# Optimization experiments

Hardware: AMD Instinct MI355X
Metric: run time of the kernel (lower is better)

Reference implementation:

```python
import jax, jax.numpy as jnp
import numpy as np

QMAX = 127.0

def quantize_mat(mat):
    # per-row (last-dim) absmax scale, kept in fp16 like the torch code,
    # truncating cast to int8 (XLA float->int convert truncates toward zero, same as torch .to(int8))
    max_val = (jnp.max(jnp.abs(mat), axis=-1) / QMAX).astype(jnp.float16)
    q = (mat / max_val[..., None]).astype(jnp.int8)
    return q, max_val


def setup_inputs() -> dict:
    key = jax.random.key(0)
    k1, k2, k3, k4 = jax.random.split(key, 4)
    B, S, IN, OUT = 8, 4096, 2048, 2048
    x = jax.random.normal(k1, (B, S, IN), dtype=jnp.float16)
    ori_w = jax.random.normal(k2, (OUT, IN), dtype=jnp.float16)
    # SmoothQuant scales: positive, bounded away from 0 (torch clamps min=1e-5)
    scales = (jax.random.uniform(k3, (IN,), dtype=jnp.float16) + jnp.float16(0.5))
    bias = jax.random.normal(k4, (OUT,), dtype=jnp.float16)
    return {"x": x, "ori_w": ori_w, "scales": scales, "bias": bias}


def reference(x, ori_w, scales, bias):
    dtype = x.dtype
    # __init__-time: smooth the weight then quantize per output row
    w = (ori_w * scales).astype(dtype)                 # [OUT, IN]
    weight_q, w_max = quantize_mat(w)                  # int8 [OUT, IN], fp16 [OUT]
    weight_qt = weight_q.T                             # stored transposed [IN, OUT]
    # forward: smooth + quantize activations
    x = (x / scales).astype(dtype)                     # [B, S, IN]
    x_q, x_max = quantize_mat(x)                       # int8 [B,S,IN], fp16 [B,S]
    res_q = jnp.matmul(x_q.astype(jnp.float32), weight_qt.astype(jnp.float32))  # [B,S,OUT]
    # dequant factor: outer product of activation and weight scales (fp16 linear, then fp32)
    mx = (x_max[..., None] * w_max).astype(jnp.float32)  # [B,S,OUT]
    res = (res_q * mx).astype(dtype)
    res = res + bias
    return res
```

## Files before the change

kernel.cpp:

```cpp
#include <hip/hip_runtime.h>
#include <hip/hip_bf16.h>
#include <cstdint>
#include <cstddef>

#define M_TOT 32768
#define N_OUT 2048
#define K_IN  2048

typedef int v4i __attribute__((ext_vector_type(4)));

__device__ __forceinline__ void gload16(const int8_t* g, int8_t* l) {
  __builtin_amdgcn_global_load_lds(
      (const __attribute__((address_space(1))) void*)g,
      (__attribute__((address_space(3))) void*)l, 16, 0, 0);
}

__global__ __launch_bounds__(256) void quant_rows_kernel(
    const float* __restrict__ in,
    const float* __restrict__ scales,
    int8_t* __restrict__ q, float* __restrict__ rmax, int mul_mode)
{
  const int row = blockIdx.x;
  const int tid = threadIdx.x;
  const size_t base = (size_t)row * K_IN + tid * 8;
  const float4 xv0 = *(const float4*)(in + base);
  const float4 xv1 = *(const float4*)(in + base + 4);
  const float4 sv0 = *(const float4*)(scales + tid * 8);
  const float4 sv1 = *(const float4*)(scales + tid * 8 + 4);
  const float xf[8] = {xv0.x, xv0.y, xv0.z, xv0.w, xv1.x, xv1.y, xv1.z, xv1.w};
  const float sf[8] = {sv0.x, sv0.y, sv0.z, sv0.w, sv1.x, sv1.y, sv1.z, sv1.w};
  _Float16 xs[8];
  float amax = 0.f;
#pragma unroll
  for (int i = 0; i < 8; ++i) {
    const _Float16 hx = (_Float16)xf[i];
    const _Float16 hs = (_Float16)sf[i];
    xs[i] = mul_mode ? (_Float16)(hx * hs) : (_Float16)(hx / hs);
    amax = fmaxf(amax, fabsf((float)xs[i]));
  }
#pragma unroll
  for (int off = 32; off; off >>= 1) amax = fmaxf(amax, __shfl_down(amax, off));
  __shared__ float red[4];
  const int wid = tid >> 6, lane = tid & 63;
  if (lane == 0) red[wid] = amax;
  __syncthreads();
  amax = fmaxf(fmaxf(red[0], red[1]), fmaxf(red[2], red[3]));
  _Float16 hqm = (_Float16)amax / (_Float16)127.0f;
  if (tid == 0) rmax[row] = (float)hqm;
  if (hqm == (_Float16)0.f) hqm = (_Float16)1.0f;
  int8_t qb[8];
#pragma unroll
  for (int i = 0; i < 8; ++i) {
    const float qf = (float)(_Float16)(xs[i] / hqm);
    qb[i] = (int8_t)(int)qf;
  }
  unsigned long long pk;
  __builtin_memcpy(&pk, qb, 8);
  *(unsigned long long*)(q + (size_t)row * K_IN + tid * 8) = pk;
}

__global__ __launch_bounds__(256) void gemm_i8_kernel(
    const int8_t* __restrict__ Aq, const int8_t* __restrict__ Bq,
    const float* __restrict__ Am, const float* __restrict__ Bm,
    const float* __restrict__ bias, float* __restrict__ out)
{
  __shared__ int8_t sA[128 * 64];
  __shared__ int8_t sB[128 * 64];
  const int tid = threadIdx.x;
  const int wid = tid >> 6, lane = tid & 63;
  const int wm = wid >> 1, wn = wid & 1;
  const long bm = (long)blockIdx.y * 128;
  const long bn = (long)blockIdx.x * 128;

  const int srow = wid * 32 + (lane >> 2);
  const int scol = (((lane & 3) ^ ((lane >> 3) & 3))) * 16;
  const int8_t* ga = Aq + (bm + srow) * K_IN + scol;
  const int8_t* gb = Bq + (bn + srow) * K_IN + scol;
  int8_t* lA = sA + wid * 2048;
  int8_t* lB = sB + wid * 2048;

  const int fr = lane & 15, fq = lane >> 4;
  const int fp = (fq ^ ((fr >> 1) & 3)) * 16;
  const int8_t* ra = sA + (wm * 64 + fr) * 64 + fp;
  const int8_t* rb = sB + (wn * 64 + fr) * 64 + fp;

  v4i acc[4][4] = {};

  for (int kt = 0; kt < K_IN; kt += 64) {
    __syncthreads();
    gload16(ga + kt,             lA);
    gload16(ga + 16 * K_IN + kt, lA + 1024);
    gload16(gb + kt,             lB);
    gload16(gb + 16 * K_IN + kt, lB + 1024);
    __syncthreads();
    v4i a[4], b[4];
#pragma unroll
    for (int i = 0; i < 4; ++i) a[i] = *(const v4i*)(ra + i * 16 * 64);
#pragma unroll
    for (int i = 0; i < 4; ++i) b[i] = *(const v4i*)(rb + i * 16 * 64);
#pragma unroll
    for (int mi = 0; mi < 4; ++mi)
#pragma unroll
      for (int ni = 0; ni < 4; ++ni)
        acc[mi][ni] = __builtin_amdgcn_mfma_i32_16x16x64_i8(a[mi], b[ni], acc[mi][ni], 0, 0, 0);
  }

  const long cm0 = bm + wm * 64;
  const int  cn0 = (int)bn + wn * 64;
  float amv[4][4];
#pragma unroll
  for (int mi = 0; mi < 4; ++mi)
#pragma unroll
    for (int r = 0; r < 4; ++r)
      amv[mi][r] = Am[cm0 + mi * 16 + fq * 4 + r];
#pragma unroll
  for (int ni = 0; ni < 4; ++ni) {
    const int col = cn0 + ni * 16 + fr;
    const float wmv = Bm[col];
    const _Float16 bsv = (_Float16)bias[col];
#pragma unroll
    for (int mi = 0; mi < 4; ++mi) {
#pragma unroll
      for (int r = 0; r < 4; ++r) {
        const long row = cm0 + mi * 16 + fq * 4 + r;
        const float mx = (float)(_Float16)((_Float16)amv[mi][r] * (_Float16)wmv);
        const _Float16 resh = (_Float16)((float)acc[mi][ni][r] * mx);
        out[row * N_OUT + col] = (float)(_Float16)(resh + bsv);
      }
    }
  }
}

extern "C" void kernel_launch(void* const* d_in, const int* in_sizes, int n_in,
                              void* d_out, int out_size, void* d_ws, size_t ws_size,
                              hipStream_t stream) {
  const float* x      = (const float*)d_in[0];
  const float* ori_w  = (const float*)d_in[1];
  const float* scales = (const float*)d_in[2];
  const float* bias   = (const float*)d_in[3];
  float* out = (float*)d_out;

  int8_t* xq = (int8_t*)d_ws;
  int8_t* wq = xq + (size_t)M_TOT * K_IN;
  float*  xm = (float*)(wq + (size_t)N_OUT * K_IN);
  float*  wmx = xm + M_TOT;

  quant_rows_kernel<<<M_TOT, 256, 0, stream>>>(x, scales, xq, xm, 0);
  quant_rows_kernel<<<N_OUT, 256, 0, stream>>>(ori_w, scales, wq, wmx, 1);

  dim3 grid(N_OUT / 128, M_TOT / 128);
  gemm_i8_kernel<<<grid, 256, 0, stream>>>(xq, wq, xm, wmx, bias, out);
}
```

Before: 636.0 us.

## Rewrite int8 GEMM with 256x256 tiles and multi-stage LDS pipeline

```diff
diff --git a/kernel.cpp b/kernel.cpp
--- a/kernel.cpp
+++ b/kernel.cpp
@@ -59,57 +59,95 @@
   *(unsigned long long*)(q + (size_t)row * K_IN + tid * 8) = pk;
 }
 
-__global__ __launch_bounds__(256) void gemm_i8_kernel(
+__global__ __launch_bounds__(512, 2) void gemm_i8_kernel(
     const int8_t* __restrict__ Aq, const int8_t* __restrict__ Bq,
     const float* __restrict__ Am, const float* __restrict__ Bm,
     const float* __restrict__ bias, float* __restrict__ out)
 {
-  __shared__ int8_t sA[128 * 64];
-  __shared__ int8_t sB[128 * 64];
+  __shared__ __align__(16) int8_t lds[8 * 16384];
   const int tid = threadIdx.x;
-  const int wid = tid >> 6, lane = tid & 63;
-  const int wm = wid >> 1, wn = wid & 1;
-  const long bm = (long)blockIdx.y * 128;
-  const long bn = (long)blockIdx.x * 128;
+  const int w = tid >> 6, lane = tid & 63;
+  const int wm = w >> 2, wn = w & 3;
+  const int bx = blockIdx.x & 7;
+  const int by = blockIdx.x >> 3;
+  const long bm = (long)by * 256;
+  const int  bn = bx * 256;
 
-  const int srow = wid * 32 + (lane >> 2);
-  const int scol = (((lane & 3) ^ ((lane >> 3) & 3))) * 16;
-  const int8_t* ga = Aq + (bm + srow) * K_IN + scol;
-  const int8_t* gb = Bq + (bn + srow) * K_IN + scol;
-  int8_t* lA = sA + wid * 2048;
-  int8_t* lB = sB + wid * 2048;
+  const int schunk = ((lane & 3) ^ ((lane >> 3) & 3)) * 16;
+  const int srow = w * 16 + (lane >> 2);
+  const int8_t* gA = Aq + (bm + srow) * (long)K_IN + schunk;
+  const int8_t* gB = Bq + ((long)(bn + srow)) * K_IN + schunk;
 
   const int fr = lane & 15, fq = lane >> 4;
-  const int fp = (fq ^ ((fr >> 1) & 3)) * 16;
-  const int8_t* ra = sA + (wm * 64 + fr) * 64 + fp;
-  const int8_t* rb = sB + (wn * 64 + fr) * 64 + fp;
+  const int pc = (fq ^ ((fr >> 1) & 3)) * 16;
+  const int aoff = (wm * 128 + fr) * 64 + pc;
+  const int boff = (wn * 64  + fr) * 64 + pc;
 
-  v4i acc[4][4] = {};
+  v4i acc[8][4] = {};
+  v4i bfr[4];
 
-  for (int kt = 0; kt < K_IN; kt += 64) {
-    __syncthreads();
-    gload16(ga + kt,             lA);
-    gload16(ga + 16 * K_IN + kt, lA + 1024);
-    gload16(gb + kt,             lB);
-    gload16(gb + 16 * K_IN + kt, lB + 1024);
-    __syncthreads();
-    v4i a[4], b[4];
+#define STAGE(G) do {                                                         \
+    const int g_ = (G);                                                       \
+    const long koff_ = (long)((g_ >> 2) * 128 + ((g_ >> 1) & 1) * 64);        \
+    int8_t* const ld_ = lds + (g_ & 7) * 16384 + w * 1024;                    \
+    const int8_t* const gp_ = (g_ & 1) ? gB : gA;                             \
+    gload16(gp_ + koff_,                  ld_);                               \
+    gload16(gp_ + koff_ + 128L * K_IN,    ld_ + 8192);                        \
+  } while (0)
+
+#define VMCNT(N) asm volatile("s_waitcnt vmcnt(" #N ")" ::: "memory")
+#define BAR() do { asm volatile("" ::: "memory");                             \
+                   __builtin_amdgcn_s_barrier();                              \
+                   asm volatile("" ::: "memory"); } while (0)
+
+#define QUAD(T, KH, MH) do {                                                  \
+    const int sa_ = (((T) & 1) * 4 + (KH) * 2) * 16384;                       \
+    if ((MH) == 0) {                                                          \
+      _Pragma("unroll")                                                       \
+      for (int ni = 0; ni < 4; ++ni)                                          \
+        bfr[ni] = *(const v4i*)(lds + sa_ + 16384 + boff + ni * 1024);        \
+    }                                                                         \
+    v4i afr[4];                                                               \
+    _Pragma("unroll")                                                         \
+    for (int mi = 0; mi < 4; ++mi)                                            \
+      afr[mi] = *(const v4i*)(lds + sa_ + aoff + ((MH) * 64 + mi * 16) * 64); \
+    __builtin_amdgcn_s_setprio(1);                                            \
+    _Pragma("unroll")                                                         \
+    for (int mi = 0; mi < 4; ++mi)                                            \
+      _Pragma("unroll")                                                       \
+      for (int ni = 0; ni < 4; ++ni)                                          \
+        acc[(MH) * 4 + mi][ni] = __builtin_amdgcn_mfma_i32_16x16x64_i8(       \
+            afr[mi], bfr[ni], acc[(MH) * 4 + mi][ni], 0, 0, 0);               \
+    __builtin_amdgcn_s_setprio(0);                                            \
+  } while (0)
+
+  STAGE(0); STAGE(1); STAGE(2); STAGE(3);
+  STAGE(4); VMCNT(8); BAR();
+
+#pragma unroll 2
+  for (int t = 0; t < 14; ++t) {
+    STAGE(4 * t + 5); VMCNT(8); BAR(); QUAD(t, 0, 0);
+    STAGE(4 * t + 6); VMCNT(8); BAR(); QUAD(t, 0, 1);
+    STAGE(4 * t + 7); VMCNT(8); BAR(); QUAD(t, 1, 0);
+    STAGE(4 * t + 8); VMCNT(8); BAR(); QUAD(t, 1, 1);
+  }
+  STAGE(61); VMCNT(8); BAR(); QUAD(14, 0, 0);
+  STAGE(62); VMCNT(8); BAR(); QUAD(14, 0, 1);
+  STAGE(63); VMCNT(8); BAR(); QUAD(14, 1, 0);
+  VMCNT(0);  BAR();
+  QUAD(14, 1, 1);
+  QUAD(15, 0, 0); QUAD(15, 0, 1); QUAD(15, 1, 0); QUAD(15, 1, 1);
+
+#undef STAGE
+#undef VMCNT
+#undef BAR
+#undef QUAD
+
+  const long cm0 = bm + wm * 128;
+  const int  cn0 = bn + wn * 64;
+  float amv[8][4];
 #pragma unroll
-    for (int i = 0; i < 4; ++i) a[i] = *(const v4i*)(ra + i * 16 * 64);
-#pragma unroll
-    for (int i = 0; i < 4; ++i) b[i] = *(const v4i*)(rb + i * 16 * 64);
-#pragma unroll
-    for (int mi = 0; mi < 4; ++mi)
-#pragma unroll
-      for (int ni = 0; ni < 4; ++ni)
-        acc[mi][ni] = __builtin_amdgcn_mfma_i32_16x16x64_i8(a[mi], b[ni], acc[mi][ni], 0, 0, 0);
-  }
-
-  const long cm0 = bm + wm * 64;
-  const int  cn0 = (int)bn + wn * 64;
-  float amv[4][4];
-#pragma unroll
-  for (int mi = 0; mi < 4; ++mi)
+  for (int mi = 0; mi < 8; ++mi)
 #pragma unroll
     for (int r = 0; r < 4; ++r)
       amv[mi][r] = Am[cm0 + mi * 16 + fq * 4 + r];
@@ -119,7 +157,7 @@
     const float wmv = Bm[col];
     const _Float16 bsv = (_Float16)bias[col];
 #pragma unroll
-    for (int mi = 0; mi < 4; ++mi) {
+    for (int mi = 0; mi < 8; ++mi) {
 #pragma unroll
       for (int r = 0; r < 4; ++r) {
         const long row = cm0 + mi * 16 + fq * 4 + r;
@@ -148,6 +186,5 @@
   quant_rows_kernel<<<M_TOT, 256, 0, stream>>>(x, scales, xq, xm, 0);
   quant_rows_kernel<<<N_OUT, 256, 0, stream>>>(ori_w, scales, wq, wmx, 1);
 
-  dim3 grid(N_OUT / 128, M_TOT / 128);
-  gemm_i8_kernel<<<grid, 256, 0, stream>>>(xq, wq, xm, wmx, bias, out);
+  gemm_i8_kernel<<<dim3(1024), 512, 0, stream>>>(xq, wq, xm, wmx, bias, out);
 }
```

Result: faster. 593.0 us (-6.8%).
